# Kernel optimization log

Hardware: AMD Instinct MI355X
Metric: run time of the kernel (lower is better)

The kernel has to match this reference:

```python
import jax, jax.numpy as jnp
import numpy as np

NUM_CLASSES = 40
EOS_COEF = 0.1
IGNORE = 255
W_CLASS, W_MASK, W_DICE = 2.0, 5.0, 5.0
EPS = 1e-8


def setup_inputs() -> dict:
    key = jax.random.key(0)
    k1, k2, k3, k4 = jax.random.split(key, 4)
    B, Q, H, W = 4, 100, 256, 256
    pred_logits = jax.random.normal(k1, (B, Q, NUM_CLASSES + 1), dtype=jnp.float32)
    pred_masks = jax.random.normal(k2, (B, Q, H, W), dtype=jnp.float32)
    targets = jax.random.randint(k3, (B, H, W), 0, NUM_CLASSES)
    ign = jax.random.uniform(k4, (B, H, W)) < 0.05
    targets = jnp.where(ign, IGNORE, targets).astype(jnp.int32)
    return {"pred_logits": pred_logits, "pred_masks": pred_masks, "targets": targets}


def reference(pred_logits, pred_masks, targets):
    B, Q, _ = pred_logits.shape
    C = NUM_CLASSES
    f32 = jnp.float32
    valid = targets != IGNORE                      # [B,H,W]
    tgt_safe = jnp.where(valid, targets, 0)        # in-range for indexing

    # ---- loss_labels: pixel->query assignment, per-query mode label ----
    # sigmoid is monotone, so argmax over queries of raw logits == argmax of sigmoid
    assign = jnp.argmax(pred_masks, axis=1)        # [B,H,W]
    b_idx = jnp.broadcast_to(jnp.arange(B)[:, None, None], targets.shape)
    # counts[b,q,c] = #valid pixels assigned to query q with label c
    counts = jnp.zeros((B, Q, C), f32).at[b_idx, assign, tgt_safe].add(valid.astype(f32))
    has_pix = counts.sum(-1) > 0                   # [B,Q]
    # mode = argmax of counts (ties -> smallest class, matching torch.mode)
    target_classes = jnp.where(has_pix, jnp.argmax(counts, axis=-1), C)  # [B,Q]

    logp = jax.nn.log_softmax(pred_logits, axis=-1)                      # [B,Q,C+1]
    nll = -jnp.take_along_axis(logp, target_classes[..., None], axis=-1)[..., 0]
    empty_weight = jnp.ones(C + 1, f32).at[-1].set(EOS_COEF)
    # ignore_index = num_classes in the CE over classes
    ce = jnp.where(target_classes != C, nll * empty_weight[target_classes], 0.0)
    p = jnp.exp(-ce)
    loss_ce = jnp.mean((1.0 - p) ** 2 * ce)

    # ---- loss_masks: per-pixel CE over queries + per-class dice ----
    logp_pix = jax.nn.log_softmax(pred_masks, axis=1)                    # [B,Q,H,W]
    nll_pix = -jnp.take_along_axis(logp_pix, tgt_safe[:, None], axis=1)[:, 0]  # [B,H,W]
    n_valid = valid.astype(f32).sum()
    ce_mask = jnp.sum(jnp.where(valid, nll_pix, 0.0)) / jnp.maximum(n_valid, 1.0)

    sig = jax.nn.sigmoid(pred_masks)                                     # [B,Q,H,W]
    tmask = (targets[:, None] == jnp.arange(C)[None, :, None, None]).astype(f32)  # [B,C,H,W]
    vm = valid[:, None].astype(f32)                                      # [B,1,H,W]
    inter = jnp.einsum('bqhw,bchw->bqc', sig, tmask * vm)                # numerator uses valid mask
    src_sum = sig.sum(axis=(2, 3))                                       # [B,Q]
    tsum = tmask.sum(axis=(2, 3))                                        # [B,C]
    dice = 2.0 * inter / (src_sum[:, :, None] + tsum[:, None, :] + EPS)  # [B,Q,C]
    present = tsum.sum(axis=0) > 0                                       # [C]
    dice_loss = jnp.sum(jnp.where(present, 1.0 - dice.mean(axis=(0, 1)), 0.0)) / C

    combined = W_MASK * ce_mask + W_DICE * dice_loss
    return W_CLASS * loss_ce + combined
```

## Files before the change

kernel.cpp:

```cpp
#include <hip/hip_runtime.h>
#include <hip/hip_bf16.h>

constexpr int B = 4, Q = 100, C = 40, Cp1 = 41, HW = 65536;
constexpr int NPIX = B * HW;

constexpr int QT = 7;
constexpr int ROWS = B * QT;
constexpr int SEGS = 128;
constexpr int KSEG = HW / SEGS;
constexpr int BWAVES = ROWS * SEGS;
constexpr int BBLK = BWAVES / 4;

constexpr int ATHR = 256, APX = 2;
constexpr int ABLKS = NPIX / (ATHR * APX);
constexpr int ASLOT = HW / (ATHR * APX);
constexpr int QU = 5;

constexpr int GRID = BBLK + ABLKS;

constexpr int WS_WORDS = 32562;

typedef __attribute__((ext_vector_type(8))) short short8;
typedef __attribute__((ext_vector_type(4))) float f32x4;

__device__ __forceinline__ short f2bf(float f) {
    unsigned u = __float_as_uint(f);
    u += 0x7FFF + ((u >> 16) & 1);
    return (short)(u >> 16);
}

__global__ void kZ(unsigned* __restrict__ ws, int n) {
    int i = blockIdx.x * blockDim.x + threadIdx.x;
    for (; i < n; i += gridDim.x * blockDim.x) ws[i] = 0u;
}

__global__ __launch_bounds__(256) void kBig(const float* __restrict__ masks,
                                            const int* __restrict__ targets,
                                            unsigned* __restrict__ counts,
                                            unsigned* __restrict__ tsum,
                                            float* __restrict__ ce_sum,
                                            unsigned* __restrict__ n_valid,
                                            float* __restrict__ inter_ext) {
    __shared__ float smem[4 * C];
    int tid = threadIdx.x;
    int blk = blockIdx.x;
    int lane = tid & 63, wave = tid >> 6;

    if (blk < BBLK) {
        int w = blk * 4 + wave;
        int row = w >> 7;
        int seg = w & (SEGS - 1);
        int b = row / QT, qt = row - b * QT;
        int q0 = qt * 16;
        int k0 = seg * KSEG;
        int m = lane & 15, quad = lane >> 4;
        int qa = q0 + m; if (qa > 99) qa = 0;
        const float* ap = masks + ((size_t)b * Q + qa) * HW + k0 + quad * 8;
        const int*   tp = targets + (size_t)b * HW + k0 + quad * 8;
        int cv0 = m, cv1 = 16 + m;
        int cv2 = (m == 8) ? 255 : 32 + m;

        f32x4 acc0 = {0.f, 0.f, 0.f, 0.f};
        f32x4 acc1 = {0.f, 0.f, 0.f, 0.f};
        f32x4 acc2 = {0.f, 0.f, 0.f, 0.f};

        #pragma unroll 2
        for (int step = 0; step < KSEG / 32; ++step) {
            int k = step * 32;
            float4 x0 = *(const float4*)(ap + k);
            float4 x1 = *(const float4*)(ap + k + 4);
            int4 t0 = *(const int4*)(tp + k);
            int4 t1 = *(const int4*)(tp + k + 4);
            float xs[8] = {x0.x, x0.y, x0.z, x0.w, x1.x, x1.y, x1.z, x1.w};
            int tss[8] = {t0.x, t0.y, t0.z, t0.w, t1.x, t1.y, t1.z, t1.w};
            short8 av, b0, b1, b2;
            #pragma unroll
            for (int j = 0; j < 8; ++j) {
                float sg = __builtin_amdgcn_rcpf(1.f + __expf(-xs[j]));
                av[j] = f2bf(sg);
                b0[j] = (tss[j] == cv0) ? (short)0x3F80 : (short)0;
                b1[j] = (tss[j] == cv1) ? (short)0x3F80 : (short)0;
                b2[j] = (tss[j] == cv2) ? (short)0x3F80 : (short)0;
            }
            acc0 = __builtin_amdgcn_mfma_f32_16x16x32_bf16(av, b0, acc0, 0, 0, 0);
            acc1 = __builtin_amdgcn_mfma_f32_16x16x32_bf16(av, b1, acc1, 0, 0, 0);
            acc2 = __builtin_amdgcn_mfma_f32_16x16x32_bf16(av, b2, acc2, 0, 0, 0);
        }

        int bq0 = b * Q + q0;
        #pragma unroll
        for (int reg = 0; reg < 4; ++reg) {
            int q = q0 + quad * 4 + reg;
            if (q < 100) {
                size_t base = (size_t)(b * Q + q) * Cp1;
                atomicAdd(&inter_ext[base + m], acc0[reg]);
                atomicAdd(&inter_ext[base + 16 + m], acc1[reg]);
                if (m <= 8) atomicAdd(&inter_ext[base + 32 + m], acc2[reg]);
            }
        }
    } else {
        unsigned* ts_local = (unsigned*)&smem[0];
        float*    cred     = &smem[64];
        unsigned* vred     = (unsigned*)&smem[72];

        int ablk = blk - BBLK;
        int b = ablk / ASLOT;
        int hw = (ablk % ASLOT) * (ATHR * APX) + tid * APX;
        const float* mp = masks + (size_t)b * Q * HW + hw;
        int2 tg = *(const int2*)(targets + (size_t)b * HW + hw);
        int tgs[2] = {tg.x, tg.y};

        float m2[2] = {-INFINITY, -INFINITY}, s[2] = {0.f, 0.f}, xt[2] = {0.f, 0.f};
        int amax[2] = {0, 0};

        for (int qq = 0; qq < Q; qq += QU) {
            float2 vv[QU];
            #pragma unroll
            for (int u = 0; u < QU; ++u)
                vv[u] = *(const float2*)(mp + (size_t)(qq + u) * HW);
            #pragma unroll
            for (int u = 0; u < QU; ++u) {
                int q = qq + u;
                float v[2] = {vv[u].x, vv[u].y};
                #pragma unroll
                for (int j = 0; j < 2; ++j) {
                    s[j] += __expf(v[j]);
                    amax[j] = (v[j] > m2[j]) ? q : amax[j];
                    m2[j] = fmaxf(m2[j], v[j]);
                    xt[j] = (q == tgs[j]) ? v[j] : xt[j];
                }
            }
        }

        if (tid < C) ts_local[tid] = 0u;
        __syncthreads();

        float ce = 0.f;
        unsigned nv = 0;
        #pragma unroll
        for (int j = 0; j < 2; ++j) {
            if (tgs[j] != 255) {
                ce += __logf(s[j]) - xt[j];
                nv++;
                atomicAdd(&counts[((size_t)b * Q + amax[j]) * C + tgs[j]], 1u);
                atomicAdd(&ts_local[tgs[j]], 1u);
            }
        }
        for (int off = 32; off; off >>= 1) {
            ce += __shfl_xor(ce, off);
            nv += __shfl_xor(nv, off);
        }
        if (lane == 0) { cred[wave] = ce; vred[wave] = nv; }
        __syncthreads();
        if (tid == 0) {
            atomicAdd(ce_sum, cred[0] + cred[1] + cred[2] + cred[3]);
            atomicAdd(n_valid, vred[0] + vred[1] + vred[2] + vred[3]);
        }
        if (tid < C) {
            unsigned t = ts_local[tid];
            if (t) atomicAdd(&tsum[b * C + tid], t);
        }
    }
}

__global__ __launch_bounds__(512) void kC(const float* __restrict__ logits,
                                          const unsigned* __restrict__ counts,
                                          const unsigned* __restrict__ tsum,
                                          const float* __restrict__ inter_ext,
                                          const float* __restrict__ ce_sum,
                                          const unsigned* __restrict__ n_valid,
                                          float* __restrict__ out) {
    int tid = threadIdx.x;
    __shared__ float dice_sum[C];
    __shared__ float ssum[B * Q];
    __shared__ float wred[8];
    __shared__ float s_lce;
    if (tid < C) dice_sum[tid] = 0.f;
    if (tid < B * Q) {
        const float* r = inter_ext + (size_t)tid * Cp1;
        float t = 0.f;
        #pragma unroll
        for (int c = 0; c < Cp1; ++c) t += r[c];
        ssum[tid] = t;
    }

    float ce_acc = 0.f;
    for (int i = tid; i < B * Q; i += 512) {
        const unsigned* cnt = counts + (size_t)i * C;
        unsigned best = 0;
        int tc = C;
        #pragma unroll
        for (int c = 0; c < C; ++c) {
            unsigned v = cnt[c];
            if (v > best) { best = v; tc = c; }
        }
        if (tc != C) {
            const float* lg = logits + (size_t)i * Cp1;
            float mm = -INFINITY, xt = 0.f;
            #pragma unroll
            for (int c = 0; c < Cp1; ++c) {
                float v = lg[c];
                mm = fmaxf(mm, v);
                if (c == tc) xt = v;
            }
            float ss = 0.f;
            #pragma unroll
            for (int c = 0; c < Cp1; ++c) ss += __expf(lg[c] - mm);
            float nll = mm + __logf(ss) - xt;
            float p = __expf(-nll);
            float om = 1.f - p;
            ce_acc += om * om * nll;
        }
    }
    for (int off = 32; off; off >>= 1) ce_acc += __shfl_xor(ce_acc, off);
    if ((tid & 63) == 0) wred[tid >> 6] = ce_acc;
    __syncthreads();
    if (tid == 0) {
        float t = 0.f;
        for (int w = 0; w < 8; ++w) t += wred[w];
        s_lce = t;
    }

    for (int i = tid; i < B * Q * C; i += 512) {
        int bq = i / C, c = i - bq * C;
        float denom = ssum[bq] + (float)tsum[(bq / Q) * C + c] + 1e-8f;
        atomicAdd(&dice_sum[c], 2.f * inter_ext[(size_t)bq * Cp1 + c] / denom);
    }
    __syncthreads();

    if (tid == 0) {
        float dl = 0.f;
        for (int c = 0; c < C; ++c) {
            unsigned ts = tsum[c] + tsum[C + c] + tsum[2 * C + c] + tsum[3 * C + c];
            if (ts > 0) dl += 1.f - dice_sum[c] * (1.f / (B * Q));
        }
        dl *= (1.f / C);
        float ce_mask = ce_sum[0] / fmaxf((float)n_valid[0], 1.f);
        float lce = s_lce * (1.f / (B * Q));
        out[0] = 2.f * lce + 5.f * ce_mask + 5.f * dl;
    }
}

extern "C" void kernel_launch(void* const* d_in, const int* in_sizes, int n_in,
                              void* d_out, int out_size, void* d_ws, size_t ws_size,
                              hipStream_t stream) {
    const float* logits  = (const float*)d_in[0];
    const float* masks   = (const float*)d_in[1];
    const int*   targets = (const int*)d_in[2];
    float* out = (float*)d_out;

    unsigned* ws        = (unsigned*)d_ws;
    unsigned* counts    = ws;
    unsigned* tsum      = ws + 16000;
    float*    ce_sum    = (float*)(ws + 16160);
    unsigned* n_valid   = ws + 16161;
    float*    inter_ext = (float*)(ws + 16162);

    kZ<<<64, 256, 0, stream>>>(ws, WS_WORDS);
    kBig<<<GRID, 256, 0, stream>>>(masks, targets, counts, tsum, ce_sum, n_valid,
                                   inter_ext);
    kC<<<1, 512, 0, stream>>>(logits, counts, tsum, inter_ext, ce_sum, n_valid, out);
}
```

Measured before the change: 225.3 us.

## Fuse dice MFMA and per-pixel softmax/argmax into one pass over masks

Replaces the two block roles (MFMA dice blocks and per-pixel CE/argmax blocks), which each read the whole mask tensor, with one kernel where each wave owns a 256-pixel segment for all 100 queries. The wave computes sigmoid for the MFMA intersection, plus the exp-sum, argmax and target logit, then reduces these across the 16 query lanes with shuffles. This halves global reads of the 105 MB mask tensor and reuses one exp for both sigmoid and softmax. In exchange it holds 21 accumulator vectors per wave (register pressure, lower occupancy), adds per-pixel shuffle reductions and serialized per-lane atomics, and launches fewer blocks (256).

```diff
diff --git a/kernel.cpp b/kernel.cpp
--- a/kernel.cpp
+++ b/kernel.cpp
@@ -2,21 +2,13 @@
 #include <hip/hip_bf16.h>
 
 constexpr int B = 4, Q = 100, C = 40, Cp1 = 41, HW = 65536;
-constexpr int NPIX = B * HW;
-
-constexpr int QT = 7;
-constexpr int ROWS = B * QT;
-constexpr int SEGS = 128;
-constexpr int KSEG = HW / SEGS;
-constexpr int BWAVES = ROWS * SEGS;
-constexpr int BBLK = BWAVES / 4;
-
-constexpr int ATHR = 256, APX = 2;
-constexpr int ABLKS = NPIX / (ATHR * APX);
-constexpr int ASLOT = HW / (ATHR * APX);
-constexpr int QU = 5;
-
-constexpr int GRID = BBLK + ABLKS;
+
+constexpr int SEGPX = 256;
+constexpr int SEGS_PER_B = HW / SEGPX;
+constexpr int NSEG = B * SEGS_PER_B;
+constexpr int OBLK = NSEG / 4;
+constexpr int NSTEP = SEGPX / 32;
+constexpr int NQT = 7;
 
 constexpr int WS_WORDS = 32562;
 
@@ -34,131 +26,148 @@
     for (; i < n; i += gridDim.x * blockDim.x) ws[i] = 0u;
 }
 
-__global__ __launch_bounds__(256) void kBig(const float* __restrict__ masks,
+__global__ __launch_bounds__(256) void kOne(const float* __restrict__ masks,
                                             const int* __restrict__ targets,
                                             unsigned* __restrict__ counts,
                                             unsigned* __restrict__ tsum,
                                             float* __restrict__ ce_sum,
                                             unsigned* __restrict__ n_valid,
                                             float* __restrict__ inter_ext) {
-    __shared__ float smem[4 * C];
+    __shared__ unsigned ts_local[C];
+    __shared__ float cred[4];
+    __shared__ unsigned vred[4];
+
     int tid = threadIdx.x;
-    int blk = blockIdx.x;
     int lane = tid & 63, wave = tid >> 6;
-
-    if (blk < BBLK) {
-        int w = blk * 4 + wave;
-        int row = w >> 7;
-        int seg = w & (SEGS - 1);
-        int b = row / QT, qt = row - b * QT;
-        int q0 = qt * 16;
-        int k0 = seg * KSEG;
-        int m = lane & 15, quad = lane >> 4;
-        int qa = q0 + m; if (qa > 99) qa = 0;
-        const float* ap = masks + ((size_t)b * Q + qa) * HW + k0 + quad * 8;
-        const int*   tp = targets + (size_t)b * HW + k0 + quad * 8;
-        int cv0 = m, cv1 = 16 + m;
-        int cv2 = (m == 8) ? 255 : 32 + m;
-
-        f32x4 acc0 = {0.f, 0.f, 0.f, 0.f};
-        f32x4 acc1 = {0.f, 0.f, 0.f, 0.f};
-        f32x4 acc2 = {0.f, 0.f, 0.f, 0.f};
-
-        #pragma unroll 2
-        for (int step = 0; step < KSEG / 32; ++step) {
-            int k = step * 32;
-            float4 x0 = *(const float4*)(ap + k);
-            float4 x1 = *(const float4*)(ap + k + 4);
-            int4 t0 = *(const int4*)(tp + k);
-            int4 t1 = *(const int4*)(tp + k + 4);
+    int m = lane & 15, quad = lane >> 4;
+
+    int seg = blockIdx.x * 4 + wave;
+    int b = seg >> 8;
+    int k0 = (seg & 255) * SEGPX;
+
+    const int* tp = targets + (size_t)b * HW + k0 + quad * 8;
+
+    int plane[NQT];
+    #pragma unroll
+    for (int qt = 0; qt < NQT; ++qt) {
+        int qa = qt * 16 + m;
+        if (qa > 99) qa = 99;
+        plane[qt] = b * Q + qa;
+    }
+    int cv0 = m, cv1 = 16 + m;
+    int cv2 = (m == 8) ? 255 : 32 + m;
+
+    f32x4 acc[NQT][3];
+    #pragma unroll
+    for (int qt = 0; qt < NQT; ++qt)
+        #pragma unroll
+        for (int a = 0; a < 3; ++a)
+            acc[qt][a] = (f32x4){0.f, 0.f, 0.f, 0.f};
+
+    if (tid < C) ts_local[tid] = 0u;
+    __syncthreads();
+
+    float ce_acc = 0.f;
+    unsigned nv = 0;
+
+    for (int step = 0; step < NSTEP; ++step) {
+        int k = k0 + quad * 8 + step * 32;
+        int tk = step * 32;
+        int4 t0 = *(const int4*)(tp + tk);
+        int4 t1 = *(const int4*)(tp + tk + 4);
+        int tss[8] = {t0.x, t0.y, t0.z, t0.w, t1.x, t1.y, t1.z, t1.w};
+
+        short8 b0, b1, b2;
+        #pragma unroll
+        for (int j = 0; j < 8; ++j) {
+            b0[j] = (tss[j] == cv0) ? (short)0x3F80 : (short)0;
+            b1[j] = (tss[j] == cv1) ? (short)0x3F80 : (short)0;
+            b2[j] = (tss[j] == cv2) ? (short)0x3F80 : (short)0;
+        }
+
+        float sE[8], mx[8], xt[8];
+        int ix[8];
+        #pragma unroll
+        for (int j = 0; j < 8; ++j) { sE[j] = 0.f; mx[j] = -INFINITY; xt[j] = 0.f; ix[j] = 0; }
+
+        #pragma unroll
+        for (int qt = 0; qt < NQT; ++qt) {
+            const float* ap = masks + (size_t)plane[qt] * HW + k;
+            float4 x0 = *(const float4*)(ap);
+            float4 x1 = *(const float4*)(ap + 4);
             float xs[8] = {x0.x, x0.y, x0.z, x0.w, x1.x, x1.y, x1.z, x1.w};
-            int tss[8] = {t0.x, t0.y, t0.z, t0.w, t1.x, t1.y, t1.z, t1.w};
-            short8 av, b0, b1, b2;
+            int q = qt * 16 + m;
+            bool valid = (qt < 6) || (m < 4);
+            short8 av;
             #pragma unroll
             for (int j = 0; j < 8; ++j) {
-                float sg = __builtin_amdgcn_rcpf(1.f + __expf(-xs[j]));
-                av[j] = f2bf(sg);
-                b0[j] = (tss[j] == cv0) ? (short)0x3F80 : (short)0;
-                b1[j] = (tss[j] == cv1) ? (short)0x3F80 : (short)0;
-                b2[j] = (tss[j] == cv2) ? (short)0x3F80 : (short)0;
-            }
-            acc0 = __builtin_amdgcn_mfma_f32_16x16x32_bf16(av, b0, acc0, 0, 0, 0);
-            acc1 = __builtin_amdgcn_mfma_f32_16x16x32_bf16(av, b1, acc1, 0, 0, 0);
-            acc2 = __builtin_amdgcn_mfma_f32_16x16x32_bf16(av, b2, acc2, 0, 0, 0);
-        }
-
-        int bq0 = b * Q + q0;
+                float v = valid ? xs[j] : -INFINITY;
+                float e = __expf(v);
+                float sig = e * __builtin_amdgcn_rcpf(1.f + e);
+                av[j] = f2bf(sig);
+                sE[j] += e;
+                bool gt = v > mx[j];
+                ix[j] = gt ? q : ix[j];
+                mx[j] = gt ? v : mx[j];
+                xt[j] += (q == tss[j]) ? v : 0.f;
+            }
+            acc[qt][0] = __builtin_amdgcn_mfma_f32_16x16x32_bf16(av, b0, acc[qt][0], 0, 0, 0);
+            acc[qt][1] = __builtin_amdgcn_mfma_f32_16x16x32_bf16(av, b1, acc[qt][1], 0, 0, 0);
+            acc[qt][2] = __builtin_amdgcn_mfma_f32_16x16x32_bf16(av, b2, acc[qt][2], 0, 0, 0);
+        }
+
+        #pragma unroll
+        for (int j = 0; j < 8; ++j) {
+            float s = sE[j], x = xt[j], mm = mx[j];
+            int ii = ix[j];
+            #pragma unroll
+            for (int msk = 1; msk <= 8; msk <<= 1) {
+                s += __shfl_xor(s, msk);
+                x += __shfl_xor(x, msk);
+                float om = __shfl_xor(mm, msk);
+                int oi = __shfl_xor(ii, msk);
+                bool take = (om > mm) || (om == mm && oi < ii);
+                mm = take ? om : mm;
+                ii = take ? oi : ii;
+            }
+            if (m == j) {
+                int tgt = tss[j];
+                if (tgt != 255) {
+                    ce_acc += __logf(s) - x;
+                    nv++;
+                    atomicAdd(&counts[((size_t)b * Q + ii) * C + tgt], 1u);
+                    atomicAdd(&ts_local[tgt], 1u);
+                }
+            }
+        }
+    }
+
+    for (int off = 32; off; off >>= 1) {
+        ce_acc += __shfl_xor(ce_acc, off);
+        nv += __shfl_xor(nv, off);
+    }
+    if (lane == 0) { cred[wave] = ce_acc; vred[wave] = nv; }
+    __syncthreads();
+    if (tid == 0) {
+        atomicAdd(ce_sum, cred[0] + cred[1] + cred[2] + cred[3]);
+        atomicAdd(n_valid, vred[0] + vred[1] + vred[2] + vred[3]);
+    }
+    if (tid < C) {
+        unsigned t = ts_local[tid];
+        if (t) atomicAdd(&tsum[b * C + tid], t);
+    }
+
+    #pragma unroll
+    for (int qt = 0; qt < NQT; ++qt) {
         #pragma unroll
         for (int reg = 0; reg < 4; ++reg) {
-            int q = q0 + quad * 4 + reg;
+            int q = qt * 16 + quad * 4 + reg;
             if (q < 100) {
                 size_t base = (size_t)(b * Q + q) * Cp1;
-                atomicAdd(&inter_ext[base + m], acc0[reg]);
-                atomicAdd(&inter_ext[base + 16 + m], acc1[reg]);
-                if (m <= 8) atomicAdd(&inter_ext[base + 32 + m], acc2[reg]);
-            }
-        }
-    } else {
-        unsigned* ts_local = (unsigned*)&smem[0];
-        float*    cred     = &smem[64];
-        unsigned* vred     = (unsigned*)&smem[72];
-
-        int ablk = blk - BBLK;
-        int b = ablk / ASLOT;
-        int hw = (ablk % ASLOT) * (ATHR * APX) + tid * APX;
-        const float* mp = masks + (size_t)b * Q * HW + hw;
-        int2 tg = *(const int2*)(targets + (size_t)b * HW + hw);
-        int tgs[2] = {tg.x, tg.y};
-
-        float m2[2] = {-INFINITY, -INFINITY}, s[2] = {0.f, 0.f}, xt[2] = {0.f, 0.f};
-        int amax[2] = {0, 0};
-
-        for (int qq = 0; qq < Q; qq += QU) {
-            float2 vv[QU];
-            #pragma unroll
-            for (int u = 0; u < QU; ++u)
-                vv[u] = *(const float2*)(mp + (size_t)(qq + u) * HW);
-            #pragma unroll
-            for (int u = 0; u < QU; ++u) {
-                int q = qq + u;
-                float v[2] = {vv[u].x, vv[u].y};
-                #pragma unroll
-                for (int j = 0; j < 2; ++j) {
-                    s[j] += __expf(v[j]);
-                    amax[j] = (v[j] > m2[j]) ? q : amax[j];
-                    m2[j] = fmaxf(m2[j], v[j]);
-                    xt[j] = (q == tgs[j]) ? v[j] : xt[j];
-                }
-            }
-        }
-
-        if (tid < C) ts_local[tid] = 0u;
-        __syncthreads();
-
-        float ce = 0.f;
-        unsigned nv = 0;
-        #pragma unroll
-        for (int j = 0; j < 2; ++j) {
-            if (tgs[j] != 255) {
-                ce += __logf(s[j]) - xt[j];
-                nv++;
-                atomicAdd(&counts[((size_t)b * Q + amax[j]) * C + tgs[j]], 1u);
-                atomicAdd(&ts_local[tgs[j]], 1u);
-            }
-        }
-        for (int off = 32; off; off >>= 1) {
-            ce += __shfl_xor(ce, off);
-            nv += __shfl_xor(nv, off);
-        }
-        if (lane == 0) { cred[wave] = ce; vred[wave] = nv; }
-        __syncthreads();
-        if (tid == 0) {
-            atomicAdd(ce_sum, cred[0] + cred[1] + cred[2] + cred[3]);
-            atomicAdd(n_valid, vred[0] + vred[1] + vred[2] + vred[3]);
-        }
-        if (tid < C) {
-            unsigned t = ts_local[tid];
-            if (t) atomicAdd(&tsum[b * C + tid], t);
+                atomicAdd(&inter_ext[base + m], acc[qt][0][reg]);
+                atomicAdd(&inter_ext[base + 16 + m], acc[qt][1][reg]);
+                if (m <= 8) atomicAdd(&inter_ext[base + 32 + m], acc[qt][2][reg]);
+            }
         }
     }
 }
@@ -257,7 +266,7 @@
     float*    inter_ext = (float*)(ws + 16162);
 
     kZ<<<64, 256, 0, stream>>>(ws, WS_WORDS);
-    kBig<<<GRID, 256, 0, stream>>>(masks, targets, counts, tsum, ce_sum, n_valid,
+    kOne<<<OBLK, 256, 0, stream>>>(masks, targets, counts, tsum, ce_sum, n_valid,
                                    inter_ext);
     kC<<<1, 512, 0, stream>>>(logits, counts, tsum, inter_ext, ce_sum, n_valid, out);
 }
```

New measurement: 279.7 us. 24.2% more time.
